# Kernel optimization log

Measured on AMD Instinct MI355X. Metric: run time of the kernel, lower is better.

Reference implementation:

```python
import itertools
import jax, jax.numpy as jnp
import numpy as np

B, N_TOK, DIM = 256, 196, 384
H, KD, D, RES = 8, 32, 128, 14
HID = (2 * KD + D) * H  # 1536


def _build_bias_idxs():
    # Faithful reproduction of the LeViT relative-offset index table.
    points = list(itertools.product(range(RES), range(RES)))
    offsets = {}
    idxs = []
    for p1 in points:
        for p2 in points:
            off = (abs(p1[0] - p2[0]), abs(p1[1] - p2[1]))
            if off not in offsets:
                offsets[off] = len(offsets)
            idxs.append(offsets[off])
    return np.asarray(idxs, dtype=np.int64).reshape(len(points), len(points)), len(offsets)


def setup_inputs() -> dict:
    key = jax.random.key(0)
    k0, k1, k2, k3, k4, k5 = jax.random.split(key, 6)
    idxs_np, n_off = _build_bias_idxs()  # n_off == 196 for RES=14
    return {
        "x": jax.random.normal(k0, (B, N_TOK, DIM), dtype=jnp.float32),
        "Wqkv": jax.random.normal(k1, (HID, DIM), dtype=jnp.float32) * 0.02,
        "bqkv": jax.random.normal(k2, (HID,), dtype=jnp.float32) * 0.02,
        "Wproj": jax.random.normal(k3, (DIM, H * D), dtype=jnp.float32) * 0.02,
        "bproj": jax.random.normal(k4, (DIM,), dtype=jnp.float32) * 0.02,
        "ab_table": jax.random.normal(k5, (H, n_off), dtype=jnp.float32) * 0.02,
        "bias_idxs": jnp.asarray(idxs_np),  # [N, N] int64
    }


def reference(x, Wqkv, bqkv, Wproj, bproj, ab_table, bias_idxs):
    Bsz, N, _ = x.shape
    scale = KD ** -0.5
    qkv = x @ Wqkv.T + bqkv                      # [B, N, HID]
    qkv = qkv.reshape(Bsz, N, H, 2 * KD + D)
    q = qkv[..., :KD]                             # [B, N, H, KD]
    k = qkv[..., KD:2 * KD]                       # [B, N, H, KD]
    v = qkv[..., 2 * KD:]                         # [B, N, H, D]
    bias = ab_table[:, bias_idxs]                 # [H, N, N] gather
    attn = jnp.einsum("bnhk,bmhk->bhnm", q, k) * scale + bias
    attn = jax.nn.softmax(attn, axis=-1)
    out = jnp.einsum("bhnm,bmhd->bnhd", attn, v).reshape(Bsz, N, H * D)
    return out @ Wproj.T + bproj                  # [B, N, DIM]
```

## Files before the change

kernel.cpp:

```cpp
#include <hip/hip_runtime.h>
#include <math.h>

#define B_SZ 256
#define N_TOKENS 196
#define DIM 384
#define NH 8
#define QKV_ST 1536
#define HID 1536
#define CTX_ST 1024
#define VT_ST 208

typedef short s16x8_base __attribute__((ext_vector_type(8)));
typedef s16x8_base __attribute__((may_alias)) s16x8;
typedef float f32x4_base __attribute__((ext_vector_type(4)));
typedef f32x4_base __attribute__((may_alias)) f32x4;

__device__ inline unsigned short f2b(float f) {
  union { float f; unsigned int u; } v; v.f = f;
  unsigned int r = (v.u + 0x7FFFu + ((v.u >> 16) & 1u)) >> 16;
  return (unsigned short)r;
}

__global__ __launch_bounds__(256)
void cvt_f32_bf16(const float* __restrict__ in, unsigned short* __restrict__ out, int n4) {
  int i = blockIdx.x * 256 + threadIdx.x;
  const int stride = gridDim.x * 256;
  for (; i < n4; i += stride) {
    float4 v = ((const float4*)in)[i];
    ushort4 o;
    o.x = f2b(v.x); o.y = f2b(v.y); o.z = f2b(v.z); o.w = f2b(v.w);
    ((ushort4*)out)[i] = o;
  }
}

__global__ __launch_bounds__(256)
void zero_vt_pad(unsigned short* __restrict__ vt, int total) {
  int i = blockIdx.x * 256 + threadIdx.x;
  if (i < total) {
    const int c = i % 12, rr = i / 12;
    vt[(size_t)rr * VT_ST + 196 + c] = 0;
  }
}

template <int MODE>
__global__ __launch_bounds__(256)
void gemm_bf16_bt(const unsigned short* __restrict__ A,
                  const unsigned short* __restrict__ Bm,
                  const float* __restrict__ bias,
                  void* __restrict__ C, unsigned short* __restrict__ vt,
                  int M, int N, int K) {
  __shared__ unsigned short As[128][32];
  __shared__ unsigned short Bs[128][32];
  const int tid = threadIdx.x;
  const int lane = tid & 63, wave = tid >> 6;
  const int quad = lane >> 4, l15 = lane & 15;
  const int ntile = N >> 7;
  const int bx = blockIdx.x % ntile, by = blockIdx.x / ntile;
  const int row0 = by << 7, col0 = bx << 7;

  const int srow = tid >> 1, soff = (tid & 1) << 4;
  const unsigned short* Ag = A + (size_t)(row0 + srow) * K + soff;
  const unsigned short* Bg = Bm + (size_t)(col0 + srow) * K + soff;

  const int wr = (wave >> 1) << 6, wc = (wave & 1) << 6;

  f32x4 zero = {0.f, 0.f, 0.f, 0.f};
  f32x4 acc[4][4];
#pragma unroll
  for (int i = 0; i < 4; ++i)
#pragma unroll
    for (int j = 0; j < 4; ++j) acc[i][j] = zero;

  s16x8 a0 = *(const s16x8*)(Ag + 0);
  s16x8 a1 = *(const s16x8*)(Ag + 8);
  s16x8 b0 = *(const s16x8*)(Bg + 0);
  s16x8 b1 = *(const s16x8*)(Bg + 8);

  for (int k0 = 0; k0 < K; k0 += 32) {
    __syncthreads();
    *(s16x8*)&As[srow][soff] = a0;
    *(s16x8*)&As[srow][soff + 8] = a1;
    *(s16x8*)&Bs[srow][soff] = b0;
    *(s16x8*)&Bs[srow][soff + 8] = b1;
    __syncthreads();
    if (k0 + 32 < K) {
      a0 = *(const s16x8*)(Ag + k0 + 32);
      a1 = *(const s16x8*)(Ag + k0 + 40);
      b0 = *(const s16x8*)(Bg + k0 + 32);
      b1 = *(const s16x8*)(Bg + k0 + 40);
    }
    s16x8 af[4], bf[4];
#pragma unroll
    for (int i = 0; i < 4; ++i) {
      af[i] = *(const s16x8*)&As[wr + i * 16 + l15][quad * 8];
      bf[i] = *(const s16x8*)&Bs[wc + i * 16 + l15][quad * 8];
    }
#pragma unroll
    for (int i = 0; i < 4; ++i)
#pragma unroll
      for (int j = 0; j < 4; ++j)
        acc[i][j] = __builtin_amdgcn_mfma_f32_16x16x32_bf16(bf[j], af[i], acc[i][j], 0, 0, 0);
  }

#pragma unroll
  for (int j = 0; j < 4; ++j) {
    const int colb = col0 + wc + j * 16 + quad * 4;
    const f32x4 bj = *(const f32x4*)&bias[colb];
    if (MODE == 0) {
#pragma unroll
      for (int i = 0; i < 4; ++i) {
        const int row = row0 + wr + i * 16 + l15;
        f32x4 v = acc[i][j] + bj;
        *(f32x4*)((float*)C + (size_t)row * N + colb) = v;
      }
    } else {
      const int hh = colb / 192;
      const int c192 = colb - hh * 192;
      if (c192 < 64) {
#pragma unroll
        for (int i = 0; i < 4; ++i) {
          const int row = row0 + wr + i * 16 + l15;
          f32x4 v = acc[i][j] + bj;
          ushort4 o;
          o.x = f2b(v[0]); o.y = f2b(v[1]); o.z = f2b(v[2]); o.w = f2b(v[3]);
          *(ushort4*)((unsigned short*)C + (size_t)row * N + colb) = o;
        }
      } else {
        const int d = c192 - 64;
#pragma unroll
        for (int i = 0; i < 4; ++i) {
          const int row = row0 + wr + i * 16 + l15;
          const int bl = row / 196;
          const int n = row - bl * 196;
          f32x4 v = acc[i][j] + bj;
          unsigned short* vp = vt + ((size_t)((bl * 8 + hh) * 128 + d)) * VT_ST + n;
#pragma unroll
          for (int r = 0; r < 4; ++r) vp[(size_t)r * VT_ST] = f2b(v[r]);
        }
      }
    }
  }
}

template <int NT>
__device__ __forceinline__ void attn_chunk64(
    const int nbase, const unsigned short* __restrict__ qbase,
    const unsigned short* __restrict__ vgw,
    const float* __restrict__ ab_s, unsigned short* __restrict__ ctxp,
    unsigned short (*__restrict__ Pm)[232], float* __restrict__ inv_s,
    const int w, const int quad, const int l15) {
  const float scale = 0.17677669529663687f;
  f32x4 zero = {0.f, 0.f, 0.f, 0.f};

  if (w < NT) {
    const int rowt = w * 16;
    s16x8 aq = *(const s16x8*)(qbase + (size_t)(nbase + rowt + l15) * QKV_ST + quad * 8);
    f32x4 sacc[13];
#pragma unroll
    for (int j = 0; j < 13; ++j) {
      s16x8 bk = *(const s16x8*)(qbase + (size_t)(j * 16 + l15) * QKV_ST + 32 + quad * 8);
      sacc[j] = __builtin_amdgcn_mfma_f32_16x16x32_bf16(aq, bk, zero, 0, 0, 0);
    }
    int rn4[4], cn4[4];
#pragma unroll
    for (int r = 0; r < 4; ++r) {
      const int n = nbase + rowt + quad * 4 + r;
      const int nn = n < 196 ? n : 195;
      rn4[r] = nn / 14;
      cn4[r] = nn - rn4[r] * 14;
    }
    float mx[4] = {-1e30f, -1e30f, -1e30f, -1e30f};
#pragma unroll
    for (int j = 0; j < 13; ++j) {
      const int m = j * 16 + l15;
      const int mc = m < 196 ? m : 195;
      const int rm = mc / 14, cm = mc - rm * 14;
#pragma unroll
      for (int r = 0; r < 4; ++r) {
        int dr = rn4[r] - rm; dr = dr < 0 ? -dr : dr;
        int dc = cn4[r] - cm; dc = dc < 0 ? -dc : dc;
        float s = fmaf(sacc[j][r], scale, ab_s[dr * 14 + dc]);
        s = (m < 196) ? s : -1e30f;
        sacc[j][r] = s;
        mx[r] = fmaxf(mx[r], s);
      }
    }
#pragma unroll
    for (int o = 8; o > 0; o >>= 1)
#pragma unroll
      for (int r = 0; r < 4; ++r) mx[r] = fmaxf(mx[r], __shfl_xor(mx[r], o));
    float sm[4] = {0.f, 0.f, 0.f, 0.f};
#pragma unroll
    for (int j = 0; j < 13; ++j)
#pragma unroll
      for (int r = 0; r < 4; ++r) {
        float e = __expf(sacc[j][r] - mx[r]);
        sm[r] += e;
        Pm[rowt + quad * 4 + r][j * 16 + l15] = f2b(e);
      }
#pragma unroll
    for (int o = 8; o > 0; o >>= 1)
#pragma unroll
      for (int r = 0; r < 4; ++r) sm[r] += __shfl_xor(sm[r], o);
    if (l15 == 0) {
#pragma unroll
      for (int r = 0; r < 4; ++r) inv_s[rowt + quad * 4 + r] = 1.f / sm[r];
    }
  }
  __syncthreads();

  f32x4 a0[NT], a1[NT];
#pragma unroll
  for (int i = 0; i < NT; ++i) { a0[i] = zero; a1[i] = zero; }
  s16x8 va0 = *(const s16x8*)(vgw + 0);
  s16x8 va1 = *(const s16x8*)(vgw + 4 * VT_ST);
#pragma unroll
  for (int ks = 0; ks < 7; ++ks) {
    s16x8 nva0, nva1;
    if (ks < 6) {
      nva0 = *(const s16x8*)(vgw + (ks + 1) * 32);
      nva1 = *(const s16x8*)(vgw + 4 * VT_ST + (ks + 1) * 32);
    }
#pragma unroll
    for (int i = 0; i < NT; ++i) {
      s16x8 pb = *(const s16x8*)&Pm[i * 16 + l15][ks * 32 + quad * 8];
      a0[i] = __builtin_amdgcn_mfma_f32_16x16x32_bf16(va0, pb, a0[i], 0, 0, 0);
      a1[i] = __builtin_amdgcn_mfma_f32_16x16x32_bf16(va1, pb, a1[i], 0, 0, 0);
    }
    va0 = nva0; va1 = nva1;
  }

#pragma unroll
  for (int i = 0; i < NT; ++i) {
    const int n = nbase + i * 16 + l15;
    if (n < 196) {
      const float is = inv_s[i * 16 + l15];
      s16x8 o;
      o[0] = (short)f2b(a0[i][0] * is); o[1] = (short)f2b(a0[i][1] * is);
      o[2] = (short)f2b(a0[i][2] * is); o[3] = (short)f2b(a0[i][3] * is);
      o[4] = (short)f2b(a1[i][0] * is); o[5] = (short)f2b(a1[i][1] * is);
      o[6] = (short)f2b(a1[i][2] * is); o[7] = (short)f2b(a1[i][3] * is);
      *(s16x8*)(ctxp + (size_t)n * CTX_ST + w * 32 + quad * 8) = o;
    }
  }
}

__global__ __launch_bounds__(256, 4)
void attn_mfma(const unsigned short* __restrict__ qkv,
               const unsigned short* __restrict__ vt,
               const float* __restrict__ ab,
               unsigned short* __restrict__ ctx) {
  __shared__ unsigned short Pm[64][232];
  __shared__ float inv_s[64];
  __shared__ float ab_s[196];

  const int bhc = blockIdx.x;
  const int bh = bhc >> 2, chunk = bhc & 3;
  const int b = bh >> 3, h = bh & 7;
  const int tid = threadIdx.x;
  const int lane = tid & 63, w = tid >> 6;
  const int quad = lane >> 4, l15 = lane & 15;

  const unsigned short* qbase = qkv + (size_t)b * N_TOKENS * QKV_ST + h * 192;
  const int pr = (l15 & 3) + ((l15 >> 2) << 3);
  const unsigned short* vgw = vt + ((size_t)bh * 128 + w * 32 + pr) * VT_ST + quad * 8;
  unsigned short* ctxp = ctx + (size_t)b * N_TOKENS * CTX_ST + h * 128;

  if (tid < 196) ab_s[tid] = ab[h * 196 + tid];
  if (tid < 64) {
#pragma unroll
    for (int c = 208; c < 232; ++c) Pm[tid][c] = 0;
  }
  __syncthreads();

  if (chunk < 3)
    attn_chunk64<4>(chunk * 64, qbase, vgw, ab_s, ctxp, Pm, inv_s, w, quad, l15);
  else
    attn_chunk64<1>(192, qbase, vgw, ab_s, ctxp, Pm, inv_s, w, quad, l15);
}

extern "C" void kernel_launch(void* const* d_in, const int* in_sizes, int n_in,
                              void* d_out, int out_size, void* d_ws, size_t ws_size,
                              hipStream_t stream) {
  const float* x     = (const float*)d_in[0];
  const float* Wqkv  = (const float*)d_in[1];
  const float* bqkv  = (const float*)d_in[2];
  const float* Wproj = (const float*)d_in[3];
  const float* bproj = (const float*)d_in[4];
  const float* ab    = (const float*)d_in[5];
  float* out = (float*)d_out;

  const size_t szWq = 589824, szWp = 393216, szX = (size_t)B_SZ * N_TOKENS * DIM;
  const size_t QPAD = 12 * QKV_ST;
  const size_t fixedB = (szWq + szWp + szX + QPAD) * 2;
  const size_t perB = (212992ULL + 301056ULL + 200704ULL) * 2;
  int Bs = 256;
  while (Bs > 32 && fixedB + (size_t)Bs * perB > ws_size) Bs >>= 1;

  unsigned short* Wqb  = (unsigned short*)d_ws;
  unsigned short* Wpb  = Wqb + szWq;
  unsigned short* xb   = Wpb + szWp;
  unsigned short* vtb  = xb + szX;
  unsigned short* qkvb = vtb + (size_t)Bs * 212992;
  unsigned short* ctxb = qkvb + (size_t)Bs * 301056 + QPAD;

  cvt_f32_bf16<<<dim3(576), dim3(256), 0, stream>>>(Wqkv, Wqb, (int)(szWq / 4));
  cvt_f32_bf16<<<dim3(384), dim3(256), 0, stream>>>(Wproj, Wpb, (int)(szWp / 4));
  cvt_f32_bf16<<<dim3(4096), dim3(256), 0, stream>>>(x, xb, (int)(szX / 4));
  {
    const int total = Bs * 8 * 128 * 12;
    zero_vt_pad<<<dim3((total + 255) / 256), dim3(256), 0, stream>>>(vtb, total);
  }

  const int nslice = B_SZ / Bs;
  const int Ms = Bs * N_TOKENS;
  for (int s = 0; s < nslice; ++s) {
    const unsigned short* xs = xb + (size_t)s * Ms * DIM;
    float* outs = out + (size_t)s * Ms * DIM;
    gemm_bf16_bt<1><<<dim3((Ms / 128) * (HID / 128)), dim3(256), 0, stream>>>(
        xs, Wqb, bqkv, qkvb, vtb, Ms, HID, DIM);
    attn_mfma<<<dim3(Bs * 8 * 4), dim3(256), 0, stream>>>(qkvb, vtb, ab, ctxb);
    gemm_bf16_bt<0><<<dim3((Ms / 128) * (DIM / 128)), dim3(256), 0, stream>>>(
        ctxb, Wpb, bproj, outs, nullptr, Ms, DIM, CTX_ST);
  }
}
```

Before: 495.5 us.

## Double-buffer GEMM shared tiles and remap workgroups across XCDs

The GEMM's shared-memory A/B tiles become double-buffered, which removes one of the two barriers per k-step and lets the next global loads be issued before the barrier. Workgroup indices in both the GEMM and the attention kernel are remapped so consecutive logical tiles land on the same XCD, aiming for better L2 reuse of shared operand rows and columns. The cost is twice the LDS per GEMM block and a small amount of extra index arithmetic.

```diff
diff --git a/kernel.cpp b/kernel.cpp
--- a/kernel.cpp
+++ b/kernel.cpp
@@ -19,6 +19,12 @@
   union { float f; unsigned int u; } v; v.f = f;
   unsigned int r = (v.u + 0x7FFFu + ((v.u >> 16) & 1u)) >> 16;
   return (unsigned short)r;
+}
+
+__device__ inline int xcd_swizzle(int bid, int nwg) {
+  const int q = nwg >> 3, r = nwg & 7;
+  const int x = bid & 7, i = bid >> 3;
+  return (x < r ? x * (q + 1) : r * (q + 1) + (x - r) * q) + i;
 }
 
 __global__ __launch_bounds__(256)
@@ -49,13 +55,14 @@
                   const float* __restrict__ bias,
                   void* __restrict__ C, unsigned short* __restrict__ vt,
                   int M, int N, int K) {
-  __shared__ unsigned short As[128][32];
-  __shared__ unsigned short Bs[128][32];
+  __shared__ unsigned short As[2][128][32];
+  __shared__ unsigned short Bs[2][128][32];
   const int tid = threadIdx.x;
   const int lane = tid & 63, wave = tid >> 6;
   const int quad = lane >> 4, l15 = lane & 15;
   const int ntile = N >> 7;
-  const int bx = blockIdx.x % ntile, by = blockIdx.x / ntile;
+  const int wg = xcd_swizzle(blockIdx.x, gridDim.x);
+  const int bx = wg % ntile, by = wg / ntile;
   const int row0 = by << 7, col0 = bx << 7;
 
   const int srow = tid >> 1, soff = (tid & 1) << 4;
@@ -76,24 +83,27 @@
   s16x8 b0 = *(const s16x8*)(Bg + 0);
   s16x8 b1 = *(const s16x8*)(Bg + 8);
 
-  for (int k0 = 0; k0 < K; k0 += 32) {
+  const int nt = K >> 5;
+#pragma unroll 1
+  for (int t = 0; t < nt; ++t) {
+    const int buf = t & 1;
+    *(s16x8*)&As[buf][srow][soff] = a0;
+    *(s16x8*)&As[buf][srow][soff + 8] = a1;
+    *(s16x8*)&Bs[buf][srow][soff] = b0;
+    *(s16x8*)&Bs[buf][srow][soff + 8] = b1;
+    if (t + 1 < nt) {
+      const int k1 = (t + 1) << 5;
+      a0 = *(const s16x8*)(Ag + k1);
+      a1 = *(const s16x8*)(Ag + k1 + 8);
+      b0 = *(const s16x8*)(Bg + k1);
+      b1 = *(const s16x8*)(Bg + k1 + 8);
+    }
     __syncthreads();
-    *(s16x8*)&As[srow][soff] = a0;
-    *(s16x8*)&As[srow][soff + 8] = a1;
-    *(s16x8*)&Bs[srow][soff] = b0;
-    *(s16x8*)&Bs[srow][soff + 8] = b1;
-    __syncthreads();
-    if (k0 + 32 < K) {
-      a0 = *(const s16x8*)(Ag + k0 + 32);
-      a1 = *(const s16x8*)(Ag + k0 + 40);
-      b0 = *(const s16x8*)(Bg + k0 + 32);
-      b1 = *(const s16x8*)(Bg + k0 + 40);
-    }
     s16x8 af[4], bf[4];
 #pragma unroll
     for (int i = 0; i < 4; ++i) {
-      af[i] = *(const s16x8*)&As[wr + i * 16 + l15][quad * 8];
-      bf[i] = *(const s16x8*)&Bs[wc + i * 16 + l15][quad * 8];
+      af[i] = *(const s16x8*)&As[buf][wr + i * 16 + l15][quad * 8];
+      bf[i] = *(const s16x8*)&Bs[buf][wc + i * 16 + l15][quad * 8];
     }
 #pragma unroll
     for (int i = 0; i < 4; ++i)
@@ -254,7 +264,7 @@
   __shared__ float inv_s[64];
   __shared__ float ab_s[196];
 
-  const int bhc = blockIdx.x;
+  const int bhc = xcd_swizzle(blockIdx.x, gridDim.x);
   const int bh = bhc >> 2, chunk = bhc & 3;
   const int b = bh >> 3, h = bh & 7;
   const int tid = threadIdx.x;
```

Measured after the change: 446.5 us. -9.9%, faster.
